# Performance work log

Hardware: AMD Instinct MI355X
Metric: run time of the kernel (lower is better)

Reference implementation:

```python
import jax, jax.numpy as jnp
import numpy as np
from jax import lax

V = 10475
J = 55
B = 512
# Kinematic tree: hardcoded chain (parent[i] = i-1), root = 0.
PARENTS = np.concatenate([[-1], np.arange(J - 1)]).astype(np.int32)


def rodrigues(r):
    """Axis-angle (..., 3) -> rotation matrices (..., 3, 3)."""
    angle = jnp.sqrt(jnp.sum(r * r, axis=-1, keepdims=True) + 1e-12)  # (...,1)
    axis = r / angle
    s = jnp.sin(angle)[..., None]
    c = jnp.cos(angle)[..., None]
    kx, ky, kz = axis[..., 0], axis[..., 1], axis[..., 2]
    z = jnp.zeros_like(kx)
    K = jnp.stack([z, -kz, ky, kz, z, -kx, -ky, kx, z], axis=-1).reshape(r.shape[:-1] + (3, 3))
    I = jnp.eye(3, dtype=r.dtype)
    return I + s * K + (1.0 - c) * (K @ K)


def setup_inputs() -> dict:
    key = jax.random.key(0)
    ks = jax.random.split(key, 16)
    inp = {
        'shape': jax.random.normal(ks[0], (1, 10), jnp.float32),
        'body_pose': jax.random.normal(ks[1], (B, 21, 3), jnp.float32) * 0.3,
        'hand_pose': jax.random.normal(ks[2], (B, 30, 3), jnp.float32) * 0.3,
        'head_pose': jax.random.normal(ks[3], (B, 3, 3), jnp.float32) * 0.3,
        'expression': jax.random.normal(ks[4], (B, 10), jnp.float32),
        'pelvis_rotation': jax.random.normal(ks[5], (B, 3), jnp.float32) * 0.3,
        'global_translation': jax.random.normal(ks[6], (B, 3), jnp.float32),
        'v_template': jax.random.normal(ks[7], (V, 3), jnp.float32),
        'shapedirs': jax.random.normal(ks[8], (V, 3, 10), jnp.float32) * 0.01,
        'exprdirs': jax.random.normal(ks[9], (V, 3, 10), jnp.float32) * 0.01,
        'posedirs': jax.random.normal(ks[10], (486, V * 3), jnp.float32) * 0.001,
    }
    w = jax.random.uniform(ks[11], (V, J), jnp.float32)
    inp['lbs_weights'] = w / jnp.sum(w, axis=-1, keepdims=True)
    jr = jax.random.uniform(ks[12], (J, V), jnp.float32)
    inp['J_regressor'] = jr / jnp.sum(jr, axis=-1, keepdims=True)
    inp['hand_mean'] = jax.random.normal(ks[13], (2, 45), jnp.float32) * 0.1
    return inp


def reference(shape, body_pose, hand_pose, head_pose, expression, pelvis_rotation,
              global_translation, v_template, shapedirs, exprdirs, posedirs,
              lbs_weights, J_regressor, hand_mean):
    b = body_pose.shape[0]
    dtype = v_template.dtype

    # 1) shape + expression blendshapes -> (B, V, 3)
    v_shaped = (v_template[None]
                + jnp.einsum('bs,vcs->bvc', shape, shapedirs)
                + jnp.einsum('be,vce->bvc', expression, exprdirs))

    # 2) joint locations (B, J, 3)
    joints = jnp.einsum('jv,bvc->bjc', J_regressor, v_shaped)

    # 3) assemble full pose (B, 55, 3): pelvis | body(21) | head(3) | hands(30)
    hands = hand_pose.reshape(b, 90) + hand_mean.reshape(90)[None]
    full_pose = jnp.concatenate(
        [pelvis_rotation[:, None], body_pose, head_pose, hands.reshape(b, 30, 3)], axis=1)
    rotmats = rodrigues(full_pose)  # (B, J, 3, 3)

    # 4) pose blendshapes
    I3 = jnp.eye(3, dtype=dtype)
    pose_feature = (rotmats[:, 1:] - I3).reshape(b, (J - 1) * 9)  # (B, 486)
    v_posed = v_shaped + (pose_feature @ posedirs).reshape(b, V, 3)

    # 5) local joint transforms (B, J, 4, 4)
    rel_joints = joints.at[:, 1:].add(-joints[:, PARENTS[1:]])
    top = jnp.concatenate([rotmats, rel_joints[..., None]], axis=-1)  # (B,J,3,4)
    bottom = jnp.broadcast_to(
        jnp.array([0., 0., 0., 1.], dtype=dtype), (b, J, 1, 4))
    T_local = jnp.concatenate([top, bottom], axis=-2)

    # 6) compose along kinematic chain (parent[i] = i-1 -> scan)
    def step(G_prev, T_i):
        G = G_prev @ T_i  # (B,4,4)
        return G, G
    G0 = T_local[:, 0]
    _, Gs = lax.scan(step, G0, jnp.swapaxes(T_local[:, 1:], 0, 1))
    G = jnp.concatenate([G0[:, None], jnp.swapaxes(Gs, 0, 1)], axis=1)  # (B,J,4,4)

    # 7) remove rest-pose joint locations: A = G * inv(rest)
    A = G.at[..., :3, 3].add(-jnp.einsum('bjrc,bjc->bjr', G[..., :3, :3], joints))

    # 8) linear blend skinning
    T = jnp.einsum('vj,bjrc->bvrc', lbs_weights, A)  # (B,V,4,4)
    verts = jnp.einsum('bvrc,bvc->bvr', T[..., :3, :3], v_posed) + T[..., :3, 3]

    # 9) ground plane + global translation
    y_offset = -jnp.min(v_template[:, 1])
    verts = verts.at[..., 1].add(y_offset)
    verts = verts + global_translation[:, None]
    return verts
```

## Files before the change

### kernel.cpp

```cpp
#include <hip/hip_runtime.h>
#include <hip/hip_bf16.h>


typedef _Float16 f16;
typedef f16  f16x8 __attribute__((ext_vector_type(8)));
typedef f16  f16x4 __attribute__((ext_vector_type(4)));
typedef float f32x4 __attribute__((ext_vector_type(4)));

#define VN    10475
#define JN    55
#define BN    512
#define VC3   31425
#define NPAD  31488
#define VPADV 10496

#define SD_F  0
#define JS_F  31425
#define JE_F  31590
#define Y_F   33240
#define PFH_BYTE  (160*1024)
#define AH_BYTE   (768*1024)
#define VPH_BYTE  (2*1024*1024)
#define LWT_BYTE  (34*1024*1024)

#define NB_SD   123
#define NB_LWT  164
#define NB_JREG 165
#define NB_PREP (NB_SD + 1 + NB_LWT + NB_JREG)

__global__ __launch_bounds__(256) void k_prep(
    const float* __restrict__ vt, const float* __restrict__ shapedirs,
    const float* __restrict__ shape, const float* __restrict__ lw,
    const float* __restrict__ jr, const float* __restrict__ exprdirs,
    float* __restrict__ ws, f16* __restrict__ lwT)
{
    __shared__ float red[256];
    const int bb  = blockIdx.x;
    const int tid = threadIdx.x;

    if (bb < NB_SD) {
        int i = bb * 256 + tid;
        if (i < VC3) {
            float acc = vt[i];
            const float* sd = shapedirs + (size_t)i * 10;
            #pragma unroll
            for (int s = 0; s < 10; ++s) acc += shape[s] * sd[s];
            ws[SD_F + i] = acc;
        }
    } else if (bb == NB_SD) {
        float m = 3.0e38f;
        for (int v = tid; v < VN; v += 256) m = fminf(m, vt[v*3 + 1]);
        red[tid] = m;
        __syncthreads();
        for (int s = 128; s > 0; s >>= 1) {
            if (tid < s) red[tid] = fminf(red[tid], red[tid + s]);
            __syncthreads();
        }
        if (tid == 0) ws[Y_F] = -red[0];
    } else if (bb < NB_SD + 1 + NB_LWT) {
        int bx = bb - (NB_SD + 1);
        int v  = bx * 64 + (tid >> 2);
        int jg = (tid & 3) * 16;
        f16 tmp[16];
        #pragma unroll
        for (int jj = 0; jj < 16; ++jj) {
            int j = jg + jj;
            tmp[jj] = (f16)((v < VN && j < JN) ? lw[(size_t)v*JN + j] : 0.f);
        }
        int vtile = v >> 4, lv = v & 15;
        int ks = jg >> 5, q0 = (jg >> 3) & 3;
        *(f16x8*)&lwT[(size_t)vtile*1024 + ks*512 + (q0*16 + lv)*8]     = *(f16x8*)&tmp[0];
        *(f16x8*)&lwT[(size_t)vtile*1024 + ks*512 + ((q0+1)*16 + lv)*8] = *(f16x8*)&tmp[8];
    } else {
        int jb = bb - (NB_SD + 1 + NB_LWT);
        int j = jb / 3, c = jb % 3;
        float acc[11];
        #pragma unroll
        for (int i = 0; i < 11; ++i) acc[i] = 0.f;
        for (int v = tid; v < VN; v += 256) {
            float w = jr[(size_t)j * VN + v];
            float sv = vt[v*3 + c];
            const float* sd = shapedirs + (size_t)(v*3 + c) * 10;
            #pragma unroll
            for (int s = 0; s < 10; ++s) sv += shape[s] * sd[s];
            acc[10] += w * sv;
            const float* ed = exprdirs + (size_t)(v*3 + c) * 10;
            #pragma unroll
            for (int e = 0; e < 10; ++e) acc[e] += w * ed[e];
        }
        for (int i = 0; i < 11; ++i) {
            red[tid] = acc[i];
            __syncthreads();
            for (int s = 128; s > 0; s >>= 1) {
                if (tid < s) red[tid] += red[tid + s];
                __syncthreads();
            }
            if (tid == 0) {
                if (i == 10) ws[JS_F + j*3 + c] = red[0];
                else         ws[JE_F + (j*3 + c)*10 + i] = red[0];
            }
            __syncthreads();
        }
    }
}

__global__ void k_batch(const float* __restrict__ body, const float* __restrict__ hand,
                        const float* __restrict__ head, const float* __restrict__ expr,
                        const float* __restrict__ pelvis, const float* __restrict__ hand_mean,
                        const float* __restrict__ ws, f16* __restrict__ PFH,
                        f16* __restrict__ AH)
{
    int b = blockIdx.x, tid = threadIdx.x;
    __shared__ float rot[JN][9];
    __shared__ float jnt[JN][3];

    f16* AHb = AH + (size_t)b * 1024;
    #pragma unroll
    for (int i = 0; i < 16; ++i) AHb[tid + i*64] = (f16)0.f;

    if (tid < JN) {
        int j = tid;
        float r0, r1, r2;
        if (j == 0) {
            r0 = pelvis[b*3+0]; r1 = pelvis[b*3+1]; r2 = pelvis[b*3+2];
        } else if (j <= 21) {
            int o = b*63 + (j-1)*3;
            r0 = body[o]; r1 = body[o+1]; r2 = body[o+2];
        } else if (j <= 24) {
            int o = b*9 + (j-22)*3;
            r0 = head[o]; r1 = head[o+1]; r2 = head[o+2];
        } else {
            int h = (j-25)*3;
            r0 = hand[b*90+h+0] + hand_mean[h+0];
            r1 = hand[b*90+h+1] + hand_mean[h+1];
            r2 = hand[b*90+h+2] + hand_mean[h+2];
        }
        float a2  = r0*r0 + r1*r1 + r2*r2 + 1e-12f;
        float ang = sqrtf(a2);
        float inv = 1.0f / ang;
        float kx = r0*inv, ky = r1*inv, kz = r2*inv;
        float s = sinf(ang), c = cosf(ang), ic = 1.0f - c;
        rot[j][0] = c + ic*kx*kx;    rot[j][1] = ic*kx*ky - s*kz; rot[j][2] = ic*kx*kz + s*ky;
        rot[j][3] = ic*kx*ky + s*kz; rot[j][4] = c + ic*ky*ky;    rot[j][5] = ic*ky*kz - s*kx;
        rot[j][6] = ic*kx*kz - s*ky; rot[j][7] = ic*ky*kz + s*kx; rot[j][8] = c + ic*kz*kz;
        #pragma unroll
        for (int cc = 0; cc < 3; ++cc) {
            float acc = ws[JS_F + j*3 + cc];
            #pragma unroll
            for (int e = 0; e < 10; ++e)
                acc += expr[b*10 + e] * ws[JE_F + (j*3 + cc)*10 + e];
            jnt[j][cc] = acc;
        }
    }
    __syncthreads();

    #pragma unroll
    for (int i = 0; i < 8; ++i) {
        int k = tid + i*64;
        float val = 0.f;
        if (k < 486) {
            int jj = k/9 + 1, ii = k%9;
            float d = (ii == 0 || ii == 4 || ii == 8) ? 1.0f : 0.0f;
            val = rot[jj][ii] - d;
        } else if (k < 496) {
            val = expr[b*10 + (k-486)];
        }
        PFH[(size_t)((b>>4)*16 + (k>>5))*512 + (((k>>3)&3)*16 + (b&15))*8 + (k&7)] = (f16)val;
    }

    int r = tid >> 2, cc = tid & 3;
    float g = 0.f;
    if (tid < 12) g = (cc < 3) ? rot[0][r*3 + cc] : jnt[0][r];
    for (int j = 0; j < JN; ++j) {
        if (j > 0) {
            float g0 = __shfl(g, r*4+0), g1 = __shfl(g, r*4+1);
            float g2 = __shfl(g, r*4+2), g3 = __shfl(g, r*4+3);
            if (cc < 3) g = g0*rot[j][cc] + g1*rot[j][3+cc] + g2*rot[j][6+cc];
            else        g = g0*(jnt[j][0]-jnt[j-1][0]) + g1*(jnt[j][1]-jnt[j-1][1])
                          + g2*(jnt[j][2]-jnt[j-1][2]) + g3;
        }
        float h0 = __shfl(g, r*4+0), h1 = __shfl(g, r*4+1), h2 = __shfl(g, r*4+2);
        float aval = g;
        if (cc == 3) aval = g - (h0*jnt[j][0] + h1*jnt[j][1] + h2*jnt[j][2]);
        if (tid < 12)
            AHb[(j>>5)*512 + (((j>>3)&3)*16 + tid)*8 + (j&7)] = (f16)aval;
    }
}

#define BTS 520
#define LTS 72
__global__ __launch_bounds__(256, 2) void k_pose(
    const float* __restrict__ pd, const float* __restrict__ ed,
    const float* __restrict__ ws, const f16* __restrict__ PFH,
    f16* __restrict__ VPH2)
{
    __shared__ f16 SH[BN*LTS];
    __shared__ float SDl[64];
    const int t = threadIdx.x;
    const int n0 = blockIdx.x * 64;
    const int w = t >> 6, lane = t & 63, l = lane & 15, q = lane >> 4;
    f16* Bt = SH;

    if (t < 64) { int n = n0 + t; SDl[t] = (n < VC3) ? ws[SD_F + n] : 0.f; }

    {
        const int krow = t & 15, f = t >> 4;
        const int nb = n0 + f*4;
        #pragma unroll 8
        for (int it = 0; it < 32; ++it) {
            int k = krow + it*16;
            float4 vv = make_float4(0.f, 0.f, 0.f, 0.f);
            if (k < 486) {
                if (nb + 3 < VC3) vv = *(const float4*)(pd + (size_t)k*VC3 + nb);
                else {
                    float* pv = (float*)&vv;
                    for (int e = 0; e < 4; ++e)
                        if (nb + e < VC3) pv[e] = pd[(size_t)k*VC3 + nb + e];
                }
            } else if (k < 496) {
                float* pv = (float*)&vv;
                for (int e = 0; e < 4; ++e)
                    if (nb + e < VC3) pv[e] = ed[(size_t)(nb + e)*10 + (k - 486)];
            }
            int c = f*4;
            Bt[(c+0)*BTS + k] = (f16)vv.x;
            Bt[(c+1)*BTS + k] = (f16)vv.y;
            Bt[(c+2)*BTS + k] = (f16)vv.z;
            Bt[(c+3)*BTS + k] = (f16)vv.w;
        }
    }
    __syncthreads();

    f32x4 acc[4][8];
    #pragma unroll
    for (int i = 0; i < 4; ++i)
        #pragma unroll
        for (int j = 0; j < 8; ++j) acc[i][j] = (f32x4)0.f;

    for (int kc = 0; kc < 16; ++kc) {
        f16x8 af[4], bf[8];
        #pragma unroll
        for (int mt = 0; mt < 4; ++mt)
            af[mt] = *(const f16x8*)&Bt[(mt*16 + l)*BTS + kc*32 + q*8];
        #pragma unroll
        for (int nt = 0; nt < 8; ++nt)
            bf[nt] = *(const f16x8*)&PFH[(size_t)((w*8 + nt)*16 + kc)*512 + lane*8];
        #pragma unroll
        for (int mt = 0; mt < 4; ++mt)
            #pragma unroll
            for (int nt = 0; nt < 8; ++nt)
                acc[mt][nt] = __builtin_amdgcn_mfma_f32_16x16x32_f16(af[mt], bf[nt], acc[mt][nt], 0, 0, 0);
    }

    __syncthreads();
    f16* L = SH;
    #pragma unroll
    for (int mt = 0; mt < 4; ++mt)
        #pragma unroll
        for (int nt = 0; nt < 8; ++nt) {
            int b = w*128 + nt*16 + l;
            f16 pack[4];
            #pragma unroll
            for (int i = 0; i < 4; ++i) {
                int c = mt*16 + q*4 + i;
                pack[i] = (f16)(acc[mt][nt][i] + SDl[c]);
            }
            *(f16x4*)&L[b*LTS + mt*16 + q*4] = *(f16x4*)&pack[0];
        }
    __syncthreads();
    {
        const int c4 = (t & 15) * 4, bq = t >> 4;
        #pragma unroll 4
        for (int it = 0; it < 32; ++it) {
            int b = bq + 16*it;
            *(f16x4*)&VPH2[(size_t)b*NPAD + n0 + c4] = *(const f16x4*)&L[b*LTS + c4];
        }
    }
}

__global__ __launch_bounds__(256, 8) void k_lbs(
    const float* __restrict__ gt, const float* __restrict__ ws,
    const f16* __restrict__ AH, const f16* __restrict__ lwT,
    const f16* __restrict__ VPH2, float* __restrict__ out)
{
    __shared__ f16   LV[8*192];
    __shared__ float OUTS[8*192];
    const int t = threadIdx.x;
    const int v0 = blockIdx.x * 64;
    const int bbase = blockIdx.y * 8;
    const int w = t >> 6, lane = t & 63, l = lane & 15, q = lane >> 4;

    if (t < 192) {
        int bl = t / 24, c8 = t % 24;
        *(f16x8*)&LV[bl*192 + c8*8] =
            *(const f16x8*)&VPH2[(size_t)(bbase + bl)*NPAD + v0*3 + c8*8];
    }
    __syncthreads();

    f32x4 acc[2][4];
    #pragma unroll
    for (int i = 0; i < 2; ++i)
        #pragma unroll
        for (int j = 0; j < 4; ++j) acc[i][j] = (f32x4)0.f;

    #pragma unroll
    for (int ks = 0; ks < 2; ++ks) {
        f16x8 af[2], bf[4];
        #pragma unroll
        for (int nt = 0; nt < 4; ++nt)
            bf[nt] = *(const f16x8*)&lwT[(size_t)(blockIdx.x*4 + nt)*1024 + ks*512 + lane*8];
        #pragma unroll
        for (int mt = 0; mt < 2; ++mt)
            af[mt] = *(const f16x8*)&AH[(size_t)(bbase + w*2 + mt)*1024 + ks*512 + lane*8];
        #pragma unroll
        for (int mt = 0; mt < 2; ++mt)
            #pragma unroll
            for (int nt = 0; nt < 4; ++nt)
                acc[mt][nt] = __builtin_amdgcn_mfma_f32_16x16x32_f16(af[mt], bf[nt], acc[mt][nt], 0, 0, 0);
    }

    float yoff = ws[Y_F];
    #pragma unroll
    for (int mt = 0; mt < 2; ++mt) {
        int bl = w*2 + mt;
        float add = 0.f;
        if (q < 3) add = gt[(bbase + bl)*3 + q] + (q == 1 ? yoff : 0.f);
        const f16* vrow = &LV[bl*192];
        #pragma unroll
        for (int nt = 0; nt < 4; ++nt) {
            if (q < 3) {
                int o = (nt*16 + l)*3;
                float vx = (float)vrow[o], vy = (float)vrow[o+1], vz = (float)vrow[o+2];
                f32x4 T = acc[mt][nt];
                OUTS[bl*192 + o + q] = T[0]*vx + T[1]*vy + T[2]*vz + T[3] + add;
            }
        }
    }
    __syncthreads();
    #pragma unroll
    for (int pass = 0; pass < 6; ++pass) {
        int idx = pass*256 + t;
        int bl  = idx / 192;
        int c   = idx - bl*192;
        if (v0*3 + c < VC3)
            out[(size_t)(bbase + bl)*VC3 + v0*3 + c] = OUTS[idx];
    }
}

extern "C" void kernel_launch(void* const* d_in, const int* in_sizes, int n_in,
                              void* d_out, int out_size, void* d_ws, size_t ws_size,
                              hipStream_t stream)
{
    const float* shape  = (const float*)d_in[0];
    const float* body   = (const float*)d_in[1];
    const float* hand   = (const float*)d_in[2];
    const float* head   = (const float*)d_in[3];
    const float* expr   = (const float*)d_in[4];
    const float* pelvis = (const float*)d_in[5];
    const float* gtrans = (const float*)d_in[6];
    const float* vt     = (const float*)d_in[7];
    const float* shdirs = (const float*)d_in[8];
    const float* exdirs = (const float*)d_in[9];
    const float* pdirs  = (const float*)d_in[10];
    const float* lbsw   = (const float*)d_in[11];
    const float* jreg   = (const float*)d_in[12];
    const float* hmean  = (const float*)d_in[13];
    float* wsf  = (float*)d_ws;
    f16*   PFH  = (f16*)((char*)d_ws + PFH_BYTE);
    f16*   AH   = (f16*)((char*)d_ws + AH_BYTE);
    f16*   VPH2 = (f16*)((char*)d_ws + VPH_BYTE);
    f16*   lwT  = (f16*)((char*)d_ws + LWT_BYTE);
    float* out  = (float*)d_out;

    hipLaunchKernelGGL(k_prep,  dim3(NB_PREP), dim3(256), 0, stream,
                       vt, shdirs, shape, lbsw, jreg, exdirs, wsf, lwT);
    hipLaunchKernelGGL(k_batch, dim3(BN),   dim3(64),  0, stream,
                       body, hand, head, expr, pelvis, hmean, wsf, PFH, AH);
    hipLaunchKernelGGL(k_pose,  dim3(NPAD/64), dim3(256), 0, stream,
                       pdirs, exdirs, wsf, PFH, VPH2);
    hipLaunchKernelGGL(k_lbs,   dim3(VPADV/64, 8192/128), dim3(256), 0, stream,
                       gtrans, wsf, AH, lwT, VPH2, out);
}
```

Baseline: 246.3 us.

## Pre-convert posedirs to f16 MFMA layout in prep, split pose GEMM across batch

The fp32-to-f16 transpose of posedirs/exprdirs moves out of k_pose into extra k_prep blocks. Those blocks write a fragment-ordered f16 buffer, staged in the output array as scratch. k_pose then loads A fragments straight from global memory with no LDS staging and uses a second grid dimension to split the 512-row batch in half. That doubles block count and halves accumulator registers, which should raise occupancy. The cost is an extra global round-trip of the converted matrix, A fragments re-read by both batch halves, and uncoalesced direct VPH2 stores without the LDS transpose.

```diff
diff --git a/kernel.cpp b/kernel.cpp
--- a/kernel.cpp
+++ b/kernel.cpp
@@ -26,15 +26,19 @@
 #define NB_SD   123
 #define NB_LWT  164
 #define NB_JREG 165
-#define NB_PREP (NB_SD + 1 + NB_LWT + NB_JREG)
+#define NB_PDT  492
+#define NB_PREP (NB_SD + 1 + NB_LWT + NB_JREG + NB_PDT)
+
+#define BTS 520
 
 __global__ __launch_bounds__(256) void k_prep(
     const float* __restrict__ vt, const float* __restrict__ shapedirs,
     const float* __restrict__ shape, const float* __restrict__ lw,
     const float* __restrict__ jr, const float* __restrict__ exprdirs,
-    float* __restrict__ ws, f16* __restrict__ lwT)
-{
-    __shared__ float red[256];
+    const float* __restrict__ pd, const float* __restrict__ ed,
+    float* __restrict__ ws, f16* __restrict__ lwT, f16* __restrict__ PDH)
+{
+    __shared__ char SMEM[64*BTS*2];
     const int bb  = blockIdx.x;
     const int tid = threadIdx.x;
 
@@ -48,6 +52,7 @@
             ws[SD_F + i] = acc;
         }
     } else if (bb == NB_SD) {
+        float* red = (float*)SMEM;
         float m = 3.0e38f;
         for (int v = tid; v < VN; v += 256) m = fminf(m, vt[v*3 + 1]);
         red[tid] = m;
@@ -71,7 +76,8 @@
         int ks = jg >> 5, q0 = (jg >> 3) & 3;
         *(f16x8*)&lwT[(size_t)vtile*1024 + ks*512 + (q0*16 + lv)*8]     = *(f16x8*)&tmp[0];
         *(f16x8*)&lwT[(size_t)vtile*1024 + ks*512 + ((q0+1)*16 + lv)*8] = *(f16x8*)&tmp[8];
-    } else {
+    } else if (bb < NB_SD + 1 + NB_LWT + NB_JREG) {
+        float* red = (float*)SMEM;
         int jb = bb - (NB_SD + 1 + NB_LWT);
         int j = jb / 3, c = jb % 3;
         float acc[11];
@@ -84,9 +90,9 @@
             #pragma unroll
             for (int s = 0; s < 10; ++s) sv += shape[s] * sd[s];
             acc[10] += w * sv;
-            const float* ed = exprdirs + (size_t)(v*3 + c) * 10;
-            #pragma unroll
-            for (int e = 0; e < 10; ++e) acc[e] += w * ed[e];
+            const float* edp = exprdirs + (size_t)(v*3 + c) * 10;
+            #pragma unroll
+            for (int e = 0; e < 10; ++e) acc[e] += w * edp[e];
         }
         for (int i = 0; i < 11; ++i) {
             red[tid] = acc[i];
@@ -101,6 +107,46 @@
             }
             __syncthreads();
         }
+    } else {
+        f16* Bt = (f16*)SMEM;
+        int bx = bb - (NB_SD + 1 + NB_LWT + NB_JREG);
+        const int n0 = bx * 64;
+        {
+            const int krow = tid & 15, f = tid >> 4;
+            const int nb = n0 + f*4;
+            #pragma unroll 8
+            for (int it = 0; it < 32; ++it) {
+                int k = krow + it*16;
+                float4 vv = make_float4(0.f, 0.f, 0.f, 0.f);
+                if (k < 486) {
+                    if (nb + 3 < VC3) vv = *(const float4*)(pd + (size_t)k*VC3 + nb);
+                    else {
+                        float* pv = (float*)&vv;
+                        for (int e = 0; e < 4; ++e)
+                            if (nb + e < VC3) pv[e] = pd[(size_t)k*VC3 + nb + e];
+                    }
+                } else if (k < 496) {
+                    float* pv = (float*)&vv;
+                    for (int e = 0; e < 4; ++e)
+                        if (nb + e < VC3) pv[e] = ed[(size_t)(nb + e)*10 + (k - 486)];
+                }
+                int c = f*4;
+                Bt[(c+0)*BTS + k] = (f16)vv.x;
+                Bt[(c+1)*BTS + k] = (f16)vv.y;
+                Bt[(c+2)*BTS + k] = (f16)vv.z;
+                Bt[(c+3)*BTS + k] = (f16)vv.w;
+            }
+        }
+        __syncthreads();
+        const int w = tid >> 6, lane = tid & 63, l = lane & 15, q = lane >> 4;
+        #pragma unroll
+        for (int mt = 0; mt < 4; ++mt)
+            #pragma unroll
+            for (int kk = 0; kk < 4; ++kk) {
+                int kc = w*4 + kk;
+                f16x8 vv8 = *(const f16x8*)&Bt[(mt*16 + l)*BTS + kc*32 + q*8];
+                *(f16x8*)&PDH[(size_t)(4*bx + mt)*8192 + kc*512 + lane*8] = vv8;
+            }
     }
 }
 
@@ -187,93 +233,52 @@
     }
 }
 
-#define BTS 520
-#define LTS 72
-__global__ __launch_bounds__(256, 2) void k_pose(
-    const float* __restrict__ pd, const float* __restrict__ ed,
-    const float* __restrict__ ws, const f16* __restrict__ PFH,
-    f16* __restrict__ VPH2)
-{
-    __shared__ f16 SH[BN*LTS];
-    __shared__ float SDl[64];
+__global__ __launch_bounds__(256) void k_pose(
+    const float* __restrict__ ws, const f16* __restrict__ PDH,
+    const f16* __restrict__ PFH, f16* __restrict__ VPH2)
+{
     const int t = threadIdx.x;
-    const int n0 = blockIdx.x * 64;
+    const int bx = blockIdx.x;
+    const int by = blockIdx.y;
+    const int n0 = bx * 64;
     const int w = t >> 6, lane = t & 63, l = lane & 15, q = lane >> 4;
-    f16* Bt = SH;
-
-    if (t < 64) { int n = n0 + t; SDl[t] = (n < VC3) ? ws[SD_F + n] : 0.f; }
-
-    {
-        const int krow = t & 15, f = t >> 4;
-        const int nb = n0 + f*4;
-        #pragma unroll 8
-        for (int it = 0; it < 32; ++it) {
-            int k = krow + it*16;
-            float4 vv = make_float4(0.f, 0.f, 0.f, 0.f);
-            if (k < 486) {
-                if (nb + 3 < VC3) vv = *(const float4*)(pd + (size_t)k*VC3 + nb);
-                else {
-                    float* pv = (float*)&vv;
-                    for (int e = 0; e < 4; ++e)
-                        if (nb + e < VC3) pv[e] = pd[(size_t)k*VC3 + nb + e];
-                }
-            } else if (k < 496) {
-                float* pv = (float*)&vv;
-                for (int e = 0; e < 4; ++e)
-                    if (nb + e < VC3) pv[e] = ed[(size_t)(nb + e)*10 + (k - 486)];
-            }
-            int c = f*4;
-            Bt[(c+0)*BTS + k] = (f16)vv.x;
-            Bt[(c+1)*BTS + k] = (f16)vv.y;
-            Bt[(c+2)*BTS + k] = (f16)vv.z;
-            Bt[(c+3)*BTS + k] = (f16)vv.w;
-        }
-    }
-    __syncthreads();
-
-    f32x4 acc[4][8];
+
+    f32x4 acc[4][4];
     #pragma unroll
     for (int i = 0; i < 4; ++i)
         #pragma unroll
-        for (int j = 0; j < 8; ++j) acc[i][j] = (f32x4)0.f;
+        for (int j = 0; j < 4; ++j) acc[i][j] = (f32x4)0.f;
 
     for (int kc = 0; kc < 16; ++kc) {
-        f16x8 af[4], bf[8];
+        f16x8 af[4], bf[4];
         #pragma unroll
         for (int mt = 0; mt < 4; ++mt)
-            af[mt] = *(const f16x8*)&Bt[(mt*16 + l)*BTS + kc*32 + q*8];
-        #pragma unroll
-        for (int nt = 0; nt < 8; ++nt)
-            bf[nt] = *(const f16x8*)&PFH[(size_t)((w*8 + nt)*16 + kc)*512 + lane*8];
+            af[mt] = *(const f16x8*)&PDH[(size_t)(4*bx + mt)*8192 + kc*512 + lane*8];
+        #pragma unroll
+        for (int nt = 0; nt < 4; ++nt)
+            bf[nt] = *(const f16x8*)&PFH[(size_t)((by*16 + w*4 + nt)*16 + kc)*512 + lane*8];
         #pragma unroll
         for (int mt = 0; mt < 4; ++mt)
             #pragma unroll
-            for (int nt = 0; nt < 8; ++nt)
+            for (int nt = 0; nt < 4; ++nt)
                 acc[mt][nt] = __builtin_amdgcn_mfma_f32_16x16x32_f16(af[mt], bf[nt], acc[mt][nt], 0, 0, 0);
     }
 
-    __syncthreads();
-    f16* L = SH;
-    #pragma unroll
-    for (int mt = 0; mt < 4; ++mt)
-        #pragma unroll
-        for (int nt = 0; nt < 8; ++nt) {
-            int b = w*128 + nt*16 + l;
+    #pragma unroll
+    for (int mt = 0; mt < 4; ++mt) {
+        int nb2 = n0 + mt*16 + q*4;
+        float sdv[4];
+        #pragma unroll
+        for (int i = 0; i < 4; ++i)
+            sdv[i] = (nb2 + i < VC3) ? ws[SD_F + nb2 + i] : 0.f;
+        #pragma unroll
+        for (int nt = 0; nt < 4; ++nt) {
+            int b = by*256 + w*64 + nt*16 + l;
             f16 pack[4];
             #pragma unroll
-            for (int i = 0; i < 4; ++i) {
-                int c = mt*16 + q*4 + i;
-                pack[i] = (f16)(acc[mt][nt][i] + SDl[c]);
-            }
-            *(f16x4*)&L[b*LTS + mt*16 + q*4] = *(f16x4*)&pack[0];
-        }
-    __syncthreads();
-    {
-        const int c4 = (t & 15) * 4, bq = t >> 4;
-        #pragma unroll 4
-        for (int it = 0; it < 32; ++it) {
-            int b = bq + 16*it;
-            *(f16x4*)&VPH2[(size_t)b*NPAD + n0 + c4] = *(const f16x4*)&L[b*LTS + c4];
+            for (int i = 0; i < 4; ++i)
+                pack[i] = (f16)(acc[mt][nt][i] + sdv[i]);
+            *(f16x4*)&VPH2[(size_t)b*NPAD + nb2] = *(f16x4*)&pack[0];
         }
     }
 }
@@ -370,14 +375,15 @@
     f16*   AH   = (f16*)((char*)d_ws + AH_BYTE);
     f16*   VPH2 = (f16*)((char*)d_ws + VPH_BYTE);
     f16*   lwT  = (f16*)((char*)d_ws + LWT_BYTE);
+    f16*   PDH  = (f16*)d_out;
     float* out  = (float*)d_out;
 
     hipLaunchKernelGGL(k_prep,  dim3(NB_PREP), dim3(256), 0, stream,
-                       vt, shdirs, shape, lbsw, jreg, exdirs, wsf, lwT);
+                       vt, shdirs, shape, lbsw, jreg, exdirs, pdirs, exdirs, wsf, lwT, PDH);
     hipLaunchKernelGGL(k_batch, dim3(BN),   dim3(64),  0, stream,
                        body, hand, head, expr, pelvis, hmean, wsf, PFH, AH);
-    hipLaunchKernelGGL(k_pose,  dim3(NPAD/64), dim3(256), 0, stream,
-                       pdirs, exdirs, wsf, PFH, VPH2);
+    hipLaunchKernelGGL(k_pose,  dim3(NPAD/64, 2), dim3(256), 0, stream,
+                       wsf, PDH, PFH, VPH2);
     hipLaunchKernelGGL(k_lbs,   dim3(VPADV/64, 8192/128), dim3(256), 0, stream,
                        gtrans, wsf, AH, lwT, VPH2, out);
 }
```

Result: slower. 266.8 us (+8.3%).

## Split pose GEMM over batch halves with 512-thread blocks and K staging

Applied to the files above, without the earlier changes.

Restructures the posedirs GEMM kernel: the grid gains a second dimension that splits the batch into two halves of 256, blocks grow to 512 threads (8 waves as 2x4 over columns and batch), and the K dimension is staged through shared memory in two 256-row halves. This shrinks shared memory and per-thread accumulators so more waves fit per CU and memory-latency hiding improves. In exchange, each posedirs tile is loaded and converted from global memory twice, once per batch half, and an extra barrier pair is added per K half.

```diff
diff --git a/kernel.cpp b/kernel.cpp
--- a/kernel.cpp
+++ b/kernel.cpp
@@ -84,9 +84,9 @@
             #pragma unroll
             for (int s = 0; s < 10; ++s) sv += shape[s] * sd[s];
             acc[10] += w * sv;
-            const float* ed = exprdirs + (size_t)(v*3 + c) * 10;
-            #pragma unroll
-            for (int e = 0; e < 10; ++e) acc[e] += w * ed[e];
+            const float* edp = exprdirs + (size_t)(v*3 + c) * 10;
+            #pragma unroll
+            for (int e = 0; e < 10; ++e) acc[e] += w * edp[e];
         }
         for (int i = 0; i < 11; ++i) {
             red[tid] = acc[i];
@@ -187,28 +187,37 @@
     }
 }
 
-#define BTS 520
+#define BTS2 264
 #define LTS 72
-__global__ __launch_bounds__(256, 2) void k_pose(
+__global__ __launch_bounds__(512, 4) void k_pose(
     const float* __restrict__ pd, const float* __restrict__ ed,
     const float* __restrict__ ws, const f16* __restrict__ PFH,
     f16* __restrict__ VPH2)
 {
-    __shared__ f16 SH[BN*LTS];
+    __shared__ f16 SH[256*LTS];
     __shared__ float SDl[64];
     const int t = threadIdx.x;
     const int n0 = blockIdx.x * 64;
+    const int by = blockIdx.y;
     const int w = t >> 6, lane = t & 63, l = lane & 15, q = lane >> 4;
+    const int wm = w >> 2, wb = w & 3;
     f16* Bt = SH;
 
     if (t < 64) { int n = n0 + t; SDl[t] = (n < VC3) ? ws[SD_F + n] : 0.f; }
 
-    {
-        const int krow = t & 15, f = t >> 4;
-        const int nb = n0 + f*4;
-        #pragma unroll 8
-        for (int it = 0; it < 32; ++it) {
-            int k = krow + it*16;
+    f32x4 acc[2][4];
+    #pragma unroll
+    for (int i = 0; i < 2; ++i)
+        #pragma unroll
+        for (int j = 0; j < 4; ++j) acc[i][j] = (f32x4)0.f;
+
+    const int krow = t & 31, f = t >> 5;
+    const int nb = n0 + f*4;
+
+    for (int h = 0; h < 2; ++h) {
+        #pragma unroll
+        for (int it = 0; it < 8; ++it) {
+            int k = h*256 + krow + it*32;
             float4 vv = make_float4(0.f, 0.f, 0.f, 0.f);
             if (k < 486) {
                 if (nb + 3 < VC3) vv = *(const float4*)(pd + (size_t)k*VC3 + nb);
@@ -222,58 +231,53 @@
                 for (int e = 0; e < 4; ++e)
                     if (nb + e < VC3) pv[e] = ed[(size_t)(nb + e)*10 + (k - 486)];
             }
-            int c = f*4;
-            Bt[(c+0)*BTS + k] = (f16)vv.x;
-            Bt[(c+1)*BTS + k] = (f16)vv.y;
-            Bt[(c+2)*BTS + k] = (f16)vv.z;
-            Bt[(c+3)*BTS + k] = (f16)vv.w;
-        }
-    }
-    __syncthreads();
-
-    f32x4 acc[4][8];
-    #pragma unroll
-    for (int i = 0; i < 4; ++i)
-        #pragma unroll
-        for (int j = 0; j < 8; ++j) acc[i][j] = (f32x4)0.f;
-
-    for (int kc = 0; kc < 16; ++kc) {
-        f16x8 af[4], bf[8];
-        #pragma unroll
-        for (int mt = 0; mt < 4; ++mt)
-            af[mt] = *(const f16x8*)&Bt[(mt*16 + l)*BTS + kc*32 + q*8];
-        #pragma unroll
-        for (int nt = 0; nt < 8; ++nt)
-            bf[nt] = *(const f16x8*)&PFH[(size_t)((w*8 + nt)*16 + kc)*512 + lane*8];
-        #pragma unroll
-        for (int mt = 0; mt < 4; ++mt)
-            #pragma unroll
-            for (int nt = 0; nt < 8; ++nt)
-                acc[mt][nt] = __builtin_amdgcn_mfma_f32_16x16x32_f16(af[mt], bf[nt], acc[mt][nt], 0, 0, 0);
-    }
-
-    __syncthreads();
+            int kl = krow + it*32;
+            Bt[(f*4+0)*BTS2 + kl] = (f16)vv.x;
+            Bt[(f*4+1)*BTS2 + kl] = (f16)vv.y;
+            Bt[(f*4+2)*BTS2 + kl] = (f16)vv.z;
+            Bt[(f*4+3)*BTS2 + kl] = (f16)vv.w;
+        }
+        __syncthreads();
+        #pragma unroll
+        for (int kc8 = 0; kc8 < 8; ++kc8) {
+            int kc = h*8 + kc8;
+            f16x8 af[2], bf[4];
+            #pragma unroll
+            for (int mt = 0; mt < 2; ++mt)
+                af[mt] = *(const f16x8*)&Bt[(wm*32 + mt*16 + l)*BTS2 + kc8*32 + q*8];
+            #pragma unroll
+            for (int nt = 0; nt < 4; ++nt)
+                bf[nt] = *(const f16x8*)&PFH[(size_t)((by*16 + wb*4 + nt)*16 + kc)*512 + lane*8];
+            #pragma unroll
+            for (int mt = 0; mt < 2; ++mt)
+                #pragma unroll
+                for (int nt = 0; nt < 4; ++nt)
+                    acc[mt][nt] = __builtin_amdgcn_mfma_f32_16x16x32_f16(af[mt], bf[nt], acc[mt][nt], 0, 0, 0);
+        }
+        __syncthreads();
+    }
+
     f16* L = SH;
     #pragma unroll
-    for (int mt = 0; mt < 4; ++mt)
-        #pragma unroll
-        for (int nt = 0; nt < 8; ++nt) {
-            int b = w*128 + nt*16 + l;
+    for (int mt = 0; mt < 2; ++mt)
+        #pragma unroll
+        for (int nt = 0; nt < 4; ++nt) {
+            int bl = wb*64 + nt*16 + l;
             f16 pack[4];
             #pragma unroll
             for (int i = 0; i < 4; ++i) {
-                int c = mt*16 + q*4 + i;
+                int c = wm*32 + mt*16 + q*4 + i;
                 pack[i] = (f16)(acc[mt][nt][i] + SDl[c]);
             }
-            *(f16x4*)&L[b*LTS + mt*16 + q*4] = *(f16x4*)&pack[0];
+            *(f16x4*)&L[bl*LTS + wm*32 + mt*16 + q*4] = *(f16x4*)&pack[0];
         }
     __syncthreads();
     {
         const int c4 = (t & 15) * 4, bq = t >> 4;
-        #pragma unroll 4
-        for (int it = 0; it < 32; ++it) {
-            int b = bq + 16*it;
-            *(f16x4*)&VPH2[(size_t)b*NPAD + n0 + c4] = *(const f16x4*)&L[b*LTS + c4];
+        #pragma unroll
+        for (int it = 0; it < 8; ++it) {
+            int bl = bq + 32*it;
+            *(f16x4*)&VPH2[(size_t)(by*256 + bl)*NPAD + n0 + c4] = *(const f16x4*)&L[bl*LTS + c4];
         }
     }
 }
@@ -376,7 +380,7 @@
                        vt, shdirs, shape, lbsw, jreg, exdirs, wsf, lwT);
     hipLaunchKernelGGL(k_batch, dim3(BN),   dim3(64),  0, stream,
                        body, hand, head, expr, pelvis, hmean, wsf, PFH, AH);
-    hipLaunchKernelGGL(k_pose,  dim3(NPAD/64), dim3(256), 0, stream,
+    hipLaunchKernelGGL(k_pose,  dim3(NPAD/64, 2), dim3(512), 0, stream,
                        pdirs, exdirs, wsf, PFH, VPH2);
     hipLaunchKernelGGL(k_lbs,   dim3(VPADV/64, 8192/128), dim3(256), 0, stream,
                        gtrans, wsf, AH, lwT, VPH2, out);
```

Result: no change. 248.0 us (+0.7%).
